# Performance work log

Measured on AMD Instinct MI355X. Metric: run time of the kernel, lower is better.

## Reference

```python
import jax, jax.numpy as jnp
import numpy as np

Y, Z, H, R = 32, 64, 256, 256  # y_dim, z_dim, h_dim, rnn_dim
T, B = 200, 2048


def setup_inputs() -> dict:
    key = jax.random.key(0)
    ks = jax.random.split(key, 32)
    w = lambda k, shape: jax.random.normal(k, shape, jnp.float32) * 0.05
    z32 = lambda n: jnp.zeros((n,), jnp.float32)
    return {
        "states": jax.random.normal(ks[0], (T, B, Y), jnp.float32),
        "eps": jax.random.normal(ks[1], (T - 1, B, Z), jnp.float32),
        # encoder q(z|x,y,h): Linear(2Y+R,H) ReLU Linear(H,H) ReLU
        "enc_w1": w(ks[2], (H, 2 * Y + R)), "enc_b1": z32(H),
        "enc_w2": w(ks[3], (H, H)), "enc_b2": z32(H),
        "enc_mw": w(ks[4], (Z, H)), "enc_mb": z32(Z),
        "enc_sw": w(ks[5], (Z, H)), "enc_sb": z32(Z),
        # prior p(z|y,h): Linear(Y+R,H) ReLU Linear(H,H) ReLU
        "pri_w1": w(ks[6], (H, Y + R)), "pri_b1": z32(H),
        "pri_w2": w(ks[7], (H, H)), "pri_b2": z32(H),
        "pri_mw": w(ks[8], (Z, H)), "pri_mb": z32(Z),
        "pri_sw": w(ks[9], (Z, H)), "pri_sb": z32(Z),
        # decoder p(x|y,z,h): Linear(Y+Z+R,H) ReLU Linear(H,H) ReLU
        "dec_w1": w(ks[10], (H, Y + Z + R)), "dec_b1": z32(H),
        "dec_w2": w(ks[11], (H, H)), "dec_b2": z32(H),
        "dec_mw": w(ks[12], (Y, H)), "dec_mb": z32(Y),
        "dec_sw": w(ks[13], (Y, H)), "dec_sb": z32(Y),
        # GRU(Y+Z -> R), 1 layer; torch gate order [r, z, n]
        "gru_wih": w(ks[14], (3 * R, Y + Z)), "gru_whh": w(ks[15], (3 * R, R)),
        "gru_bih": z32(3 * R), "gru_bhh": z32(3 * R),
    }


def reference(states, eps, enc_w1, enc_b1, enc_w2, enc_b2, enc_mw, enc_mb,
              enc_sw, enc_sb, pri_w1, pri_b1, pri_w2, pri_b2, pri_mw, pri_mb,
              pri_sw, pri_sb, dec_w1, dec_b1, dec_w2, dec_b2, dec_mw, dec_mb,
              dec_sw, dec_sb, gru_wih, gru_whh, gru_bih, gru_bhh):
    batch = states.shape[1]
    rnn_dim = gru_whh.shape[1]
    relu, sp = jax.nn.relu, jax.nn.softplus
    LOG2PI = jnp.float32(np.log(2.0 * np.pi))

    def mlp2(x, w1, b1, w2, b2):
        return relu(relu(x @ w1.T + b1) @ w2.T + b2)

    def step(h, inp):
        y, x, e = inp  # y=states[t], x=states[t+1], e: reparam noise
        enc_h = mlp2(jnp.concatenate([x, y, h], 1), enc_w1, enc_b1, enc_w2, enc_b2)
        em = enc_h @ enc_mw.T + enc_mb
        es = sp(enc_h @ enc_sw.T + enc_sb)
        pri_h = mlp2(jnp.concatenate([y, h], 1), pri_w1, pri_b1, pri_w2, pri_b2)
        pm = pri_h @ pri_mw.T + pri_mb
        ps = sp(pri_h @ pri_sw.T + pri_sb)
        z = em + es * e  # sample_gauss
        dec_h = mlp2(jnp.concatenate([y, z, h], 1), dec_w1, dec_b1, dec_w2, dec_b2)
        dm = dec_h @ dec_mw.T + dec_mb
        ds = sp(dec_h @ dec_sw.T + dec_sb)
        # GRU cell (torch gate order r,z,n)
        gi = jnp.concatenate([x, z], 1) @ gru_wih.T + gru_bih
        gh = h @ gru_whh.T + gru_bhh
        ir, iz, inn = jnp.split(gi, 3, axis=1)
        hr, hz, hn = jnp.split(gh, 3, axis=1)
        r = jax.nn.sigmoid(ir + hr)
        u = jax.nn.sigmoid(iz + hz)
        n = jnp.tanh(inn + r * hn)
        h_new = (1.0 - u) * n + u * h
        kl = 0.5 * jnp.sum(2.0 * jnp.log(ps / es) + (es ** 2 + (em - pm) ** 2) / ps ** 2 - 1.0)
        nll = jnp.sum(jnp.log(ds) + (x - dm) ** 2 / (2.0 * ds ** 2) + 0.5 * LOG2PI)
        return h_new, (kl, nll)

    h0 = jnp.zeros((batch, rnn_dim), states.dtype)
    _, (kls, nlls) = jax.lax.scan(step, h0, (states[:-1], states[1:], eps))
    # out = [kl_loss, recon_loss]
    return jnp.stack([jnp.sum(kls), jnp.sum(nlls)])
```

## Files before the change

kernel.cpp:

```cpp
#include <hip/hip_runtime.h>

typedef unsigned short u16;
typedef unsigned int u32;
typedef __bf16 bf16x8 __attribute__((ext_vector_type(8)));
typedef float f32x4 __attribute__((ext_vector_type(4)));

#define YD 32
#define ZD 64
#define HD 256
#define RD 256
#define TSTEPS 199
#define BB 2048
#define MROWS 32
#define NBLK 64
#define NTHR 1024
#define CATS 392
#define HBS  264
#define HES  136
#define HDS  72

enum : int {
  OFF_ENC_W1 = 0,
  OFF_ENC_W2 = 81920,
  OFF_ENC_H  = 147456,
  OFF_PRI_W1 = 180224,
  OFF_PRI_W2 = 253952,
  OFF_PRI_H  = 319488,
  OFF_DEC_W1 = 352256,
  OFF_DEC_W2 = 442368,
  OFF_DEC_H  = 507904,
  OFF_GWIH   = 524288,
  OFF_GWHH   = 598016,
};

__device__ __forceinline__ u16 f2bf(float f) {
  u32 u = __float_as_uint(f);
  u += 0x7fffu + ((u >> 16) & 1u);
  return (u16)(u >> 16);
}
__device__ __forceinline__ float bf2f(u16 b) {
  return __uint_as_float((u32)b << 16);
}
__device__ __forceinline__ float softplus_f(float x) {
  float l = __logf(1.f + __expf(-fabsf(x)));
  return x > 0.f ? x + l : l;
}
__device__ __forceinline__ float sigmoid_f(float x) {
  return __builtin_amdgcn_rcpf(1.f + __expf(-x));
}
__device__ __forceinline__ float tanh_f(float x) {
  float e = __expf(-2.f * fabsf(x));
  float t = (1.f - e) * __builtin_amdgcn_rcpf(1.f + e);
  return x >= 0.f ? t : -t;
}

template<int NT, int RT, int KS, int AS>
__device__ __forceinline__ void gemm_seg(f32x4 (&acc)[NT][RT],
    const u16* __restrict__ W, const int Kw, const int wrow0, const int wk0,
    const u16* A, const int acol0, const int rt0, const int lane)
{
  const int n = lane & 15, quad = lane >> 4;
  bf16x8 b[KS][NT];
  #pragma unroll
  for (int nt = 0; nt < NT; ++nt) {
    const u16* wp = W + (size_t)(wrow0 + nt * 16 + n) * Kw + wk0 + quad * 8;
    #pragma unroll
    for (int ks = 0; ks < KS; ++ks)
      b[ks][nt] = *reinterpret_cast<const bf16x8*>(wp + ks * 32);
  }
  #pragma unroll
  for (int ks = 0; ks < KS; ++ks) {
    bf16x8 a[RT];
    #pragma unroll
    for (int rt = 0; rt < RT; ++rt)
      a[rt] = *reinterpret_cast<const bf16x8*>(A + ((rt0 + rt) * 16 + n) * AS + acol0 + ks * 32 + quad * 8);
    #pragma unroll
    for (int nt = 0; nt < NT; ++nt)
      #pragma unroll
      for (int rt = 0; rt < RT; ++rt)
        acc[nt][rt] = __builtin_amdgcn_mfma_f32_16x16x32_bf16(a[rt], b[ks][nt], acc[nt][rt], 0, 0, 0);
  }
}

template<int RT, int DS>
__device__ __forceinline__ void store_relu(const f32x4 (&acc)[1][RT], u16* dst,
    const int col0, const int rt0, const float bias, const int lane)
{
  const int n = lane & 15, quad = lane >> 4;
  #pragma unroll
  for (int rt = 0; rt < RT; ++rt)
    #pragma unroll
    for (int i = 0; i < 4; ++i) {
      float v = fmaxf(acc[0][rt][i] + bias, 0.f);
      dst[((rt0 + rt) * 16 + quad * 4 + i) * DS + col0 + n] = f2bf(v);
    }
}

struct PrepArgs { const float* src[14]; int off[14]; int cnt[14]; };

__global__ void prep_weights(PrepArgs a, u16* __restrict__ dst) {
  const int j = blockIdx.y;
  const float* __restrict__ s = a.src[j];
  u16* d = dst + a.off[j];
  const int nel = a.cnt[j];
  for (int i = blockIdx.x * blockDim.x + threadIdx.x; i < nel; i += gridDim.x * blockDim.x)
    d[i] = f2bf(s[i]);
}

__global__ void zero_out_k(float* out) { if (threadIdx.x < 2) out[threadIdx.x] = 0.f; }

__global__ __launch_bounds__(NTHR, 4)
void vrnn_kernel(const float* __restrict__ states, const float* __restrict__ eps,
                 const float* __restrict__ enc_b1, const float* __restrict__ enc_b2,
                 const float* __restrict__ enc_mb, const float* __restrict__ enc_sb,
                 const float* __restrict__ pri_b1, const float* __restrict__ pri_b2,
                 const float* __restrict__ pri_mb, const float* __restrict__ pri_sb,
                 const float* __restrict__ dec_b1, const float* __restrict__ dec_b2,
                 const float* __restrict__ dec_mb, const float* __restrict__ dec_sb,
                 const float* __restrict__ gbih, const float* __restrict__ gbhh,
                 const u16* __restrict__ ws, float* __restrict__ out)
{
  __shared__ u16 cat[MROWS * CATS];
  __shared__ u16 hb1[MROWS * HBS];
  __shared__ u16 hb2[MROWS * HBS];
  __shared__ u16 hbhE[MROWS * HES];
  __shared__ u16 hbhP[MROWS * HES];
  __shared__ u16 hbhD[MROWS * HDS];

  const int tid = threadIdx.x;
  const int w = tid >> 6, lane = tid & 63;
  const int n = lane & 15, quad = lane >> 4;
  const int r0 = blockIdx.x * MROWS;
  const int n0 = w * 16;
  const int cgE = w & 7, rtE = w >> 3;
  const int cgD = w & 3, rtD = (w >> 2) & 1;

  const int jW = n0 + n;
  const float b1e = enc_b1[jW], b2e = enc_b2[jW];
  const float b1p = pri_b1[jW], b2p = pri_b2[jW];
  const float b1d = dec_b1[jW], b2d = dec_b2[jW];
  const float brg = gbih[jW] + gbhh[jW];
  const float bug = gbih[RD + jW] + gbhh[RD + jW];
  const float bing = gbih[2 * RD + jW];
  const float bhng = gbhh[2 * RD + jW];
  const float bhE = (cgE < 4) ? enc_mb[cgE * 16 + n] : enc_sb[(cgE - 4) * 16 + n];
  const float bhP = (cgE < 4) ? pri_mb[cgE * 16 + n] : pri_sb[(cgE - 4) * 16 + n];
  const float bhD = (cgD < 2) ? dec_mb[cgD * 16 + n] : dec_sb[(cgD - 2) * 16 + n];

  for (int i = tid; i < MROWS * (HD / 2); i += NTHR) {
    int row = i >> 7, c = (i & 127) * 2;
    *reinterpret_cast<u32*>(&cat[row * CATS + 128 + c]) = 0u;
  }

  float hreg[2][4];
  #pragma unroll
  for (int a = 0; a < 2; ++a)
    #pragma unroll
    for (int c = 0; c < 4; ++c) hreg[a][c] = 0.f;

  const int srow = (tid & 255) >> 3, sc4 = (tid & 7) * 4;
  float4 xyf = make_float4(0.f, 0.f, 0.f, 0.f);
  if (tid < 512)
    xyf = *reinterpret_cast<const float4*>(states + ((size_t)((tid < 256) ? 1 : 0) * BB + r0 + srow) * YD + sc4);

  const int mz = tid >> 5, jz = (tid & 31) * 2;
  const int mn = (tid & 511) >> 4, jn = (tid & 15) * 2;

  float kl_acc = 0.f, nll_acc = 0.f;

  for (int t = 0; t < TSTEPS; ++t) {
    if (tid < 512) {
      u16* d = cat + srow * CATS + ((tid < 256) ? 0 : 32) + sc4;
      d[0] = f2bf(xyf.x); d[1] = f2bf(xyf.y); d[2] = f2bf(xyf.z); d[3] = f2bf(xyf.w);
    }
    float2 ev2 = *reinterpret_cast<const float2*>(eps + ((size_t)t * BB + r0 + mz) * ZD + jz);
    float2 xs2 = make_float2(0.f, 0.f);
    if (tid < 512)
      xs2 = *reinterpret_cast<const float2*>(states + ((size_t)(t + 1) * BB + r0 + mn) * YD + jn);
    __syncthreads();

    {
      f32x4 acc[1][2] = {};
      gemm_seg<1, 2, 2, CATS>(acc, ws + OFF_ENC_W1, 320, n0, 0, cat, 0, 0, lane);
      gemm_seg<1, 2, 8, CATS>(acc, ws + OFF_ENC_W1, 320, n0, 64, cat, 128, 0, lane);
      store_relu<2, HBS>(acc, hb1, n0, 0, b1e, lane);
    }
    __syncthreads();

    {
      f32x4 acc[1][2] = {};
      gemm_seg<1, 2, 8, HBS>(acc, ws + OFF_ENC_W2, 256, n0, 0, hb1, 0, 0, lane);
      store_relu<2, HBS>(acc, hb2, n0, 0, b2e, lane);
    }
    __syncthreads();

    {
      f32x4 acc[1][1] = {};
      gemm_seg<1, 1, 8, HBS>(acc, ws + OFF_ENC_H, 256, cgE * 16, 0, hb2, 0, rtE, lane);
      #pragma unroll
      for (int i = 0; i < 4; ++i) {
        float v = acc[0][0][i] + bhE;
        if (cgE >= 4) v = softplus_f(v);
        hbhE[(rtE * 16 + quad * 4 + i) * HES + cgE * 16 + n] = f2bf(v);
      }
    }
    __syncthreads();

    {
      float em0 = bf2f(hbhE[mz * HES + jz]);
      float em1 = bf2f(hbhE[mz * HES + jz + 1]);
      float es0 = bf2f(hbhE[mz * HES + 64 + jz]);
      float es1 = bf2f(hbhE[mz * HES + 64 + jz + 1]);
      cat[mz * CATS + 64 + jz] = f2bf(em0 + es0 * ev2.x);
      cat[mz * CATS + 64 + jz + 1] = f2bf(em1 + es1 * ev2.y);
      f32x4 acc[1][2] = {};
      gemm_seg<1, 2, 1, CATS>(acc, ws + OFF_PRI_W1, 288, n0, 0, cat, 32, 0, lane);
      gemm_seg<1, 2, 8, CATS>(acc, ws + OFF_PRI_W1, 288, n0, 32, cat, 128, 0, lane);
      store_relu<2, HBS>(acc, hb1, n0, 0, b1p, lane);
    }
    __syncthreads();

    {
      f32x4 acc[1][2] = {};
      gemm_seg<1, 2, 8, HBS>(acc, ws + OFF_PRI_W2, 256, n0, 0, hb1, 0, 0, lane);
      store_relu<2, HBS>(acc, hb2, n0, 0, b2p, lane);
    }
    __syncthreads();

    {
      f32x4 acc[1][1] = {};
      gemm_seg<1, 1, 8, HBS>(acc, ws + OFF_PRI_H, 256, cgE * 16, 0, hb2, 0, rtE, lane);
      #pragma unroll
      for (int i = 0; i < 4; ++i) {
        float v = acc[0][0][i] + bhP;
        if (cgE >= 4) v = softplus_f(v);
        hbhP[(rtE * 16 + quad * 4 + i) * HES + cgE * 16 + n] = f2bf(v);
      }
    }
    __syncthreads();

    {
      #pragma unroll
      for (int c = 0; c < 2; ++c) {
        float em = bf2f(hbhE[mz * HES + jz + c]);
        float es = bf2f(hbhE[mz * HES + 64 + jz + c]);
        float pm = bf2f(hbhP[mz * HES + jz + c]);
        float ps = bf2f(hbhP[mz * HES + 64 + jz + c]);
        float d = em - pm;
        kl_acc += 0.5f * (2.f * __logf(ps * __builtin_amdgcn_rcpf(es))
                          + (es * es + d * d) / (ps * ps) - 1.f);
      }
      f32x4 acc[1][2] = {};
      gemm_seg<1, 2, 3, CATS>(acc, ws + OFF_DEC_W1, 352, n0, 0, cat, 32, 0, lane);
      gemm_seg<1, 2, 8, CATS>(acc, ws + OFF_DEC_W1, 352, n0, 96, cat, 128, 0, lane);
      store_relu<2, HBS>(acc, hb1, n0, 0, b1d, lane);
    }
    __syncthreads();

    {
      f32x4 acc[1][2] = {};
      gemm_seg<1, 2, 8, HBS>(acc, ws + OFF_DEC_W2, 256, n0, 0, hb1, 0, 0, lane);
      store_relu<2, HBS>(acc, hb2, n0, 0, b2d, lane);
    }
    __syncthreads();

    {
      if (w < 8) {
        f32x4 acc[1][1] = {};
        gemm_seg<1, 1, 8, HBS>(acc, ws + OFF_DEC_H, 256, cgD * 16, 0, hb2, 0, rtD, lane);
        #pragma unroll
        for (int i = 0; i < 4; ++i) {
          float v = acc[0][0][i] + bhD;
          if (cgD >= 2) v = softplus_f(v);
          hbhD[(rtD * 16 + quad * 4 + i) * HDS + cgD * 16 + n] = f2bf(v);
        }
      }
      f32x4 aH[1][2] = {};
      gemm_seg<1, 2, 8, CATS>(aH, ws + OFF_GWHH, 256, 2 * RD + n0, 0, cat, 128, 0, lane);
      {
        f32x4 aR[1][2] = {};
        gemm_seg<1, 2, 1, CATS>(aR, ws + OFF_GWIH, 96, n0, 0, cat, 0, 0, lane);
        gemm_seg<1, 2, 2, CATS>(aR, ws + OFF_GWIH, 96, n0, 32, cat, 64, 0, lane);
        gemm_seg<1, 2, 8, CATS>(aR, ws + OFF_GWHH, 256, n0, 0, cat, 128, 0, lane);
        #pragma unroll
        for (int rt = 0; rt < 2; ++rt)
          #pragma unroll
          for (int i = 0; i < 4; ++i)
            aH[0][rt][i] = sigmoid_f(aR[0][rt][i] + brg) * (aH[0][rt][i] + bhng);
      }
      {
        f32x4 aN[1][2] = {};
        gemm_seg<1, 2, 1, CATS>(aN, ws + OFF_GWIH, 96, 2 * RD + n0, 0, cat, 0, 0, lane);
        gemm_seg<1, 2, 2, CATS>(aN, ws + OFF_GWIH, 96, 2 * RD + n0, 32, cat, 64, 0, lane);
        #pragma unroll
        for (int rt = 0; rt < 2; ++rt)
          #pragma unroll
          for (int i = 0; i < 4; ++i)
            aH[0][rt][i] = tanh_f(aN[0][rt][i] + bing + aH[0][rt][i]);
      }
      {
        f32x4 aU[1][2] = {};
        gemm_seg<1, 2, 1, CATS>(aU, ws + OFF_GWIH, 96, RD + n0, 0, cat, 0, 0, lane);
        gemm_seg<1, 2, 2, CATS>(aU, ws + OFF_GWIH, 96, RD + n0, 32, cat, 64, 0, lane);
        gemm_seg<1, 2, 8, CATS>(aU, ws + OFF_GWHH, 256, RD + n0, 0, cat, 128, 0, lane);
        #pragma unroll
        for (int rt = 0; rt < 2; ++rt)
          #pragma unroll
          for (int i = 0; i < 4; ++i) {
            float u = sigmoid_f(aU[0][rt][i] + bug);
            hreg[rt][i] = (1.f - u) * aH[0][rt][i] + u * hreg[rt][i];
          }
      }
      const int tn = (t + 1 < TSTEPS) ? t + 1 : TSTEPS - 1;
      if (tid < 512)
        xyf = *reinterpret_cast<const float4*>(states + ((size_t)((tid < 256) ? tn + 1 : tn) * BB + r0 + srow) * YD + sc4);
    }
    __syncthreads();

    if (tid < 512) {
      #pragma unroll
      for (int c = 0; c < 2; ++c) {
        float dm = bf2f(hbhD[mn * HDS + jn + c]);
        float ds = bf2f(hbhD[mn * HDS + 32 + jn + c]);
        float xv = (c == 0) ? xs2.x : xs2.y;
        float dd = xv - dm;
        nll_acc += __logf(ds) + dd * dd / (2.f * ds * ds) + 0.91893853320467274178f;
      }
    }
    #pragma unroll
    for (int rt = 0; rt < 2; ++rt)
      #pragma unroll
      for (int i = 0; i < 4; ++i)
        cat[(rt * 16 + quad * 4 + i) * CATS + 128 + n0 + n] = f2bf(hreg[rt][i]);
  }

  float kv = kl_acc, nv = nll_acc;
  #pragma unroll
  for (int off = 32; off > 0; off >>= 1) {
    kv += __shfl_down(kv, off, 64);
    nv += __shfl_down(nv, off, 64);
  }
  if (lane == 0) {
    atomicAdd(out + 0, kv);
    atomicAdd(out + 1, nv);
  }
}

extern "C" void kernel_launch(void* const* d_in, const int* in_sizes, int n_in,
                              void* d_out, int out_size, void* d_ws, size_t ws_size,
                              hipStream_t stream) {
  const float* states = (const float*)d_in[0];
  const float* eps    = (const float*)d_in[1];
  u16* ws   = (u16*)d_ws;
  float* out = (float*)d_out;

  PrepArgs pa;
  const int jsrc[14] = {2, 4, 6, 8, 10, 12, 14, 16, 18, 20, 22, 24, 26, 27};
  const int joff[14] = {OFF_ENC_W1, OFF_ENC_W2, OFF_ENC_H, OFF_ENC_H + 16384,
                        OFF_PRI_W1, OFF_PRI_W2, OFF_PRI_H, OFF_PRI_H + 16384,
                        OFF_DEC_W1, OFF_DEC_W2, OFF_DEC_H, OFF_DEC_H + 8192,
                        OFF_GWIH, OFF_GWHH};
  const int jcnt[14] = {81920, 65536, 16384, 16384,
                        73728, 65536, 16384, 16384,
                        90112, 65536, 8192, 8192,
                        73728, 196608};
  for (int j = 0; j < 14; ++j) {
    pa.src[j] = (const float*)d_in[jsrc[j]];
    pa.off[j] = joff[j];
    pa.cnt[j] = jcnt[j];
  }

  zero_out_k<<<dim3(1), dim3(64), 0, stream>>>(out);
  prep_weights<<<dim3(64, 14), dim3(256), 0, stream>>>(pa, ws);
  vrnn_kernel<<<dim3(NBLK), dim3(NTHR), 0, stream>>>(
      states, eps,
      (const float*)d_in[3],  (const float*)d_in[5],
      (const float*)d_in[7],  (const float*)d_in[9],
      (const float*)d_in[11], (const float*)d_in[13],
      (const float*)d_in[15], (const float*)d_in[17],
      (const float*)d_in[19], (const float*)d_in[21],
      (const float*)d_in[23], (const float*)d_in[25],
      (const float*)d_in[28], (const float*)d_in[29],
      ws, out);
}
```

Measured before the change: 10.77 ms.

## Process 64 batch rows per block to double weight reuse per MFMA fragment

Each block now handles 64 batch rows instead of 32, so each loaded weight fragment feeds four MFMA row tiles instead of two, halving the global/L2 weight traffic per row. Grid shrinks to 32 blocks, the LDS padding strides change, and the decoder-head buffer is folded into hb1 to fit the larger tiles in LDS. Input loads become nontemporal, and all threads now take part in staging states, eps and the NLL terms. With 32 blocks on a many-CU GPU, far fewer compute units are busy, which may outweigh the reuse gain.

```diff
diff --git a/kernel.cpp b/kernel.cpp
--- a/kernel.cpp
+++ b/kernel.cpp
@@ -4,6 +4,7 @@
 typedef unsigned int u32;
 typedef __bf16 bf16x8 __attribute__((ext_vector_type(8)));
 typedef float f32x4 __attribute__((ext_vector_type(4)));
+typedef float f32x2 __attribute__((ext_vector_type(2)));
 
 #define YD 32
 #define ZD 64
@@ -11,13 +12,12 @@
 #define RD 256
 #define TSTEPS 199
 #define BB 2048
-#define MROWS 32
-#define NBLK 64
+#define MROWS 64
+#define NBLK 32
 #define NTHR 1024
-#define CATS 392
-#define HBS  264
-#define HES  136
-#define HDS  72
+#define CATS 388
+#define HBS  260
+#define HES  132
 
 enum : int {
   OFF_ENC_W1 = 0,
@@ -54,36 +54,29 @@
   return x >= 0.f ? t : -t;
 }
 
-template<int NT, int RT, int KS, int AS>
-__device__ __forceinline__ void gemm_seg(f32x4 (&acc)[NT][RT],
+template<int RT, int KS, int AS>
+__device__ __forceinline__ void gemm_seg(f32x4 (&acc)[RT],
     const u16* __restrict__ W, const int Kw, const int wrow0, const int wk0,
     const u16* A, const int acol0, const int rt0, const int lane)
 {
   const int n = lane & 15, quad = lane >> 4;
-  bf16x8 b[KS][NT];
-  #pragma unroll
-  for (int nt = 0; nt < NT; ++nt) {
-    const u16* wp = W + (size_t)(wrow0 + nt * 16 + n) * Kw + wk0 + quad * 8;
+  bf16x8 b[KS];
+  const u16* wp = W + (size_t)(wrow0 + n) * Kw + wk0 + quad * 8;
+  #pragma unroll
+  for (int ks = 0; ks < KS; ++ks)
+    b[ks] = *reinterpret_cast<const bf16x8*>(wp + ks * 32);
+  #pragma unroll
+  for (int ks = 0; ks < KS; ++ks) {
     #pragma unroll
-    for (int ks = 0; ks < KS; ++ks)
-      b[ks][nt] = *reinterpret_cast<const bf16x8*>(wp + ks * 32);
-  }
-  #pragma unroll
-  for (int ks = 0; ks < KS; ++ks) {
-    bf16x8 a[RT];
-    #pragma unroll
-    for (int rt = 0; rt < RT; ++rt)
-      a[rt] = *reinterpret_cast<const bf16x8*>(A + ((rt0 + rt) * 16 + n) * AS + acol0 + ks * 32 + quad * 8);
-    #pragma unroll
-    for (int nt = 0; nt < NT; ++nt)
-      #pragma unroll
-      for (int rt = 0; rt < RT; ++rt)
-        acc[nt][rt] = __builtin_amdgcn_mfma_f32_16x16x32_bf16(a[rt], b[ks][nt], acc[nt][rt], 0, 0, 0);
+    for (int rt = 0; rt < RT; ++rt) {
+      bf16x8 a = *reinterpret_cast<const bf16x8*>(A + ((rt0 + rt) * 16 + n) * AS + acol0 + ks * 32 + quad * 8);
+      acc[rt] = __builtin_amdgcn_mfma_f32_16x16x32_bf16(a, b[ks], acc[rt], 0, 0, 0);
+    }
   }
 }
 
 template<int RT, int DS>
-__device__ __forceinline__ void store_relu(const f32x4 (&acc)[1][RT], u16* dst,
+__device__ __forceinline__ void store_relu(const f32x4 (&acc)[RT], u16* dst,
     const int col0, const int rt0, const float bias, const int lane)
 {
   const int n = lane & 15, quad = lane >> 4;
@@ -91,7 +84,7 @@
   for (int rt = 0; rt < RT; ++rt)
     #pragma unroll
     for (int i = 0; i < 4; ++i) {
-      float v = fmaxf(acc[0][rt][i] + bias, 0.f);
+      float v = fmaxf(acc[rt][i] + bias, 0.f);
       dst[((rt0 + rt) * 16 + quad * 4 + i) * DS + col0 + n] = f2bf(v);
     }
 }
@@ -125,15 +118,14 @@
   __shared__ u16 hb2[MROWS * HBS];
   __shared__ u16 hbhE[MROWS * HES];
   __shared__ u16 hbhP[MROWS * HES];
-  __shared__ u16 hbhD[MROWS * HDS];
 
   const int tid = threadIdx.x;
   const int w = tid >> 6, lane = tid & 63;
   const int n = lane & 15, quad = lane >> 4;
   const int r0 = blockIdx.x * MROWS;
   const int n0 = w * 16;
-  const int cgE = w & 7, rtE = w >> 3;
-  const int cgD = w & 3, rtD = (w >> 2) & 1;
+  const int cgE = w & 7, rtE0 = (w >> 3) * 2;
+  const int cgD = w & 3, rtD = w >> 2;
 
   const int jW = n0 + n;
   const float b1e = enc_b1[jW], b2e = enc_b2[jW];
@@ -152,96 +144,100 @@
     *reinterpret_cast<u32*>(&cat[row * CATS + 128 + c]) = 0u;
   }
 
-  float hreg[2][4];
-  #pragma unroll
-  for (int a = 0; a < 2; ++a)
+  float hreg[4][4];
+  #pragma unroll
+  for (int a = 0; a < 4; ++a)
     #pragma unroll
     for (int c = 0; c < 4; ++c) hreg[a][c] = 0.f;
 
-  const int srow = (tid & 255) >> 3, sc4 = (tid & 7) * 4;
-  float4 xyf = make_float4(0.f, 0.f, 0.f, 0.f);
-  if (tid < 512)
-    xyf = *reinterpret_cast<const float4*>(states + ((size_t)((tid < 256) ? 1 : 0) * BB + r0 + srow) * YD + sc4);
-
-  const int mz = tid >> 5, jz = (tid & 31) * 2;
-  const int mn = (tid & 511) >> 4, jn = (tid & 15) * 2;
+  const int srow = (tid & 511) >> 3, sc4 = (tid & 7) * 4;
+  f32x4 xyf = __builtin_nontemporal_load(
+      reinterpret_cast<const f32x4*>(states + ((size_t)((tid < 512) ? 1 : 0) * BB + r0 + srow) * YD + sc4));
+
+  const int mz = tid >> 4, jz = (tid & 15) * 4;
+  const int mn = tid >> 4, jn = (tid & 15) * 2;
 
   float kl_acc = 0.f, nll_acc = 0.f;
 
   for (int t = 0; t < TSTEPS; ++t) {
-    if (tid < 512) {
-      u16* d = cat + srow * CATS + ((tid < 256) ? 0 : 32) + sc4;
+    {
+      u16* d = cat + srow * CATS + ((tid < 512) ? 0 : 32) + sc4;
       d[0] = f2bf(xyf.x); d[1] = f2bf(xyf.y); d[2] = f2bf(xyf.z); d[3] = f2bf(xyf.w);
     }
-    float2 ev2 = *reinterpret_cast<const float2*>(eps + ((size_t)t * BB + r0 + mz) * ZD + jz);
-    float2 xs2 = make_float2(0.f, 0.f);
-    if (tid < 512)
-      xs2 = *reinterpret_cast<const float2*>(states + ((size_t)(t + 1) * BB + r0 + mn) * YD + jn);
-    __syncthreads();
-
-    {
-      f32x4 acc[1][2] = {};
-      gemm_seg<1, 2, 2, CATS>(acc, ws + OFF_ENC_W1, 320, n0, 0, cat, 0, 0, lane);
-      gemm_seg<1, 2, 8, CATS>(acc, ws + OFF_ENC_W1, 320, n0, 64, cat, 128, 0, lane);
-      store_relu<2, HBS>(acc, hb1, n0, 0, b1e, lane);
-    }
-    __syncthreads();
-
-    {
-      f32x4 acc[1][2] = {};
-      gemm_seg<1, 2, 8, HBS>(acc, ws + OFF_ENC_W2, 256, n0, 0, hb1, 0, 0, lane);
-      store_relu<2, HBS>(acc, hb2, n0, 0, b2e, lane);
-    }
-    __syncthreads();
-
-    {
-      f32x4 acc[1][1] = {};
-      gemm_seg<1, 1, 8, HBS>(acc, ws + OFF_ENC_H, 256, cgE * 16, 0, hb2, 0, rtE, lane);
-      #pragma unroll
-      for (int i = 0; i < 4; ++i) {
-        float v = acc[0][0][i] + bhE;
-        if (cgE >= 4) v = softplus_f(v);
-        hbhE[(rtE * 16 + quad * 4 + i) * HES + cgE * 16 + n] = f2bf(v);
-      }
-    }
-    __syncthreads();
-
-    {
-      float em0 = bf2f(hbhE[mz * HES + jz]);
-      float em1 = bf2f(hbhE[mz * HES + jz + 1]);
-      float es0 = bf2f(hbhE[mz * HES + 64 + jz]);
-      float es1 = bf2f(hbhE[mz * HES + 64 + jz + 1]);
-      cat[mz * CATS + 64 + jz] = f2bf(em0 + es0 * ev2.x);
-      cat[mz * CATS + 64 + jz + 1] = f2bf(em1 + es1 * ev2.y);
-      f32x4 acc[1][2] = {};
-      gemm_seg<1, 2, 1, CATS>(acc, ws + OFF_PRI_W1, 288, n0, 0, cat, 32, 0, lane);
-      gemm_seg<1, 2, 8, CATS>(acc, ws + OFF_PRI_W1, 288, n0, 32, cat, 128, 0, lane);
-      store_relu<2, HBS>(acc, hb1, n0, 0, b1p, lane);
-    }
-    __syncthreads();
-
-    {
-      f32x4 acc[1][2] = {};
-      gemm_seg<1, 2, 8, HBS>(acc, ws + OFF_PRI_W2, 256, n0, 0, hb1, 0, 0, lane);
-      store_relu<2, HBS>(acc, hb2, n0, 0, b2p, lane);
-    }
-    __syncthreads();
-
-    {
-      f32x4 acc[1][1] = {};
-      gemm_seg<1, 1, 8, HBS>(acc, ws + OFF_PRI_H, 256, cgE * 16, 0, hb2, 0, rtE, lane);
-      #pragma unroll
-      for (int i = 0; i < 4; ++i) {
-        float v = acc[0][0][i] + bhP;
-        if (cgE >= 4) v = softplus_f(v);
-        hbhP[(rtE * 16 + quad * 4 + i) * HES + cgE * 16 + n] = f2bf(v);
-      }
-    }
-    __syncthreads();
-
-    {
-      #pragma unroll
-      for (int c = 0; c < 2; ++c) {
+    f32x4 ev4 = __builtin_nontemporal_load(
+        reinterpret_cast<const f32x4*>(eps + ((size_t)t * BB + r0 + mz) * ZD + jz));
+    f32x2 xs2 = __builtin_nontemporal_load(
+        reinterpret_cast<const f32x2*>(states + ((size_t)(t + 1) * BB + r0 + mn) * YD + jn));
+    __syncthreads();
+
+    {
+      f32x4 acc[4] = {};
+      gemm_seg<4, 2, CATS>(acc, ws + OFF_ENC_W1, 320, n0, 0, cat, 0, 0, lane);
+      gemm_seg<4, 8, CATS>(acc, ws + OFF_ENC_W1, 320, n0, 64, cat, 128, 0, lane);
+      store_relu<4, HBS>(acc, hb1, n0, 0, b1e, lane);
+    }
+    __syncthreads();
+
+    {
+      f32x4 acc[4] = {};
+      gemm_seg<4, 8, HBS>(acc, ws + OFF_ENC_W2, 256, n0, 0, hb1, 0, 0, lane);
+      store_relu<4, HBS>(acc, hb2, n0, 0, b2e, lane);
+    }
+    __syncthreads();
+
+    {
+      f32x4 acc[2] = {};
+      gemm_seg<2, 8, HBS>(acc, ws + OFF_ENC_H, 256, cgE * 16, 0, hb2, 0, rtE0, lane);
+      #pragma unroll
+      for (int rt = 0; rt < 2; ++rt)
+        #pragma unroll
+        for (int i = 0; i < 4; ++i) {
+          float v = acc[rt][i] + bhE;
+          if (cgE >= 4) v = softplus_f(v);
+          hbhE[((rtE0 + rt) * 16 + quad * 4 + i) * HES + cgE * 16 + n] = f2bf(v);
+        }
+    }
+    __syncthreads();
+
+    {
+      const float e4[4] = {ev4.x, ev4.y, ev4.z, ev4.w};
+      #pragma unroll
+      for (int c = 0; c < 4; ++c) {
+        float em = bf2f(hbhE[mz * HES + jz + c]);
+        float es = bf2f(hbhE[mz * HES + 64 + jz + c]);
+        cat[mz * CATS + 64 + jz + c] = f2bf(em + es * e4[c]);
+      }
+      f32x4 acc[4] = {};
+      gemm_seg<4, 1, CATS>(acc, ws + OFF_PRI_W1, 288, n0, 0, cat, 32, 0, lane);
+      gemm_seg<4, 8, CATS>(acc, ws + OFF_PRI_W1, 288, n0, 32, cat, 128, 0, lane);
+      store_relu<4, HBS>(acc, hb1, n0, 0, b1p, lane);
+    }
+    __syncthreads();
+
+    {
+      f32x4 acc[4] = {};
+      gemm_seg<4, 8, HBS>(acc, ws + OFF_PRI_W2, 256, n0, 0, hb1, 0, 0, lane);
+      store_relu<4, HBS>(acc, hb2, n0, 0, b2p, lane);
+    }
+    __syncthreads();
+
+    {
+      f32x4 acc[2] = {};
+      gemm_seg<2, 8, HBS>(acc, ws + OFF_PRI_H, 256, cgE * 16, 0, hb2, 0, rtE0, lane);
+      #pragma unroll
+      for (int rt = 0; rt < 2; ++rt)
+        #pragma unroll
+        for (int i = 0; i < 4; ++i) {
+          float v = acc[rt][i] + bhP;
+          if (cgE >= 4) v = softplus_f(v);
+          hbhP[((rtE0 + rt) * 16 + quad * 4 + i) * HES + cgE * 16 + n] = f2bf(v);
+        }
+    }
+    __syncthreads();
+
+    {
+      #pragma unroll
+      for (int c = 0; c < 4; ++c) {
         float em = bf2f(hbhE[mz * HES + jz + c]);
         float es = bf2f(hbhE[mz * HES + 64 + jz + c]);
         float pm = bf2f(hbhP[mz * HES + jz + c]);
@@ -250,85 +246,85 @@
         kl_acc += 0.5f * (2.f * __logf(ps * __builtin_amdgcn_rcpf(es))
                           + (es * es + d * d) / (ps * ps) - 1.f);
       }
-      f32x4 acc[1][2] = {};
-      gemm_seg<1, 2, 3, CATS>(acc, ws + OFF_DEC_W1, 352, n0, 0, cat, 32, 0, lane);
-      gemm_seg<1, 2, 8, CATS>(acc, ws + OFF_DEC_W1, 352, n0, 96, cat, 128, 0, lane);
-      store_relu<2, HBS>(acc, hb1, n0, 0, b1d, lane);
-    }
-    __syncthreads();
-
-    {
-      f32x4 acc[1][2] = {};
-      gemm_seg<1, 2, 8, HBS>(acc, ws + OFF_DEC_W2, 256, n0, 0, hb1, 0, 0, lane);
-      store_relu<2, HBS>(acc, hb2, n0, 0, b2d, lane);
-    }
-    __syncthreads();
-
-    {
-      if (w < 8) {
-        f32x4 acc[1][1] = {};
-        gemm_seg<1, 1, 8, HBS>(acc, ws + OFF_DEC_H, 256, cgD * 16, 0, hb2, 0, rtD, lane);
+      f32x4 acc[4] = {};
+      gemm_seg<4, 3, CATS>(acc, ws + OFF_DEC_W1, 352, n0, 0, cat, 32, 0, lane);
+      gemm_seg<4, 8, CATS>(acc, ws + OFF_DEC_W1, 352, n0, 96, cat, 128, 0, lane);
+      store_relu<4, HBS>(acc, hb1, n0, 0, b1d, lane);
+    }
+    __syncthreads();
+
+    {
+      f32x4 acc[4] = {};
+      gemm_seg<4, 8, HBS>(acc, ws + OFF_DEC_W2, 256, n0, 0, hb1, 0, 0, lane);
+      store_relu<4, HBS>(acc, hb2, n0, 0, b2d, lane);
+    }
+    __syncthreads();
+
+    {
+      {
+        f32x4 acc[1] = {};
+        gemm_seg<1, 8, HBS>(acc, ws + OFF_DEC_H, 256, cgD * 16, 0, hb2, 0, rtD, lane);
         #pragma unroll
         for (int i = 0; i < 4; ++i) {
-          float v = acc[0][0][i] + bhD;
+          float v = acc[0][i] + bhD;
           if (cgD >= 2) v = softplus_f(v);
-          hbhD[(rtD * 16 + quad * 4 + i) * HDS + cgD * 16 + n] = f2bf(v);
+          hb1[(rtD * 16 + quad * 4 + i) * HBS + cgD * 16 + n] = f2bf(v);
         }
       }
-      f32x4 aH[1][2] = {};
-      gemm_seg<1, 2, 8, CATS>(aH, ws + OFF_GWHH, 256, 2 * RD + n0, 0, cat, 128, 0, lane);
+      f32x4 aH[4] = {};
+      gemm_seg<4, 8, CATS>(aH, ws + OFF_GWHH, 256, 2 * RD + n0, 0, cat, 128, 0, lane);
       {
-        f32x4 aR[1][2] = {};
-        gemm_seg<1, 2, 1, CATS>(aR, ws + OFF_GWIH, 96, n0, 0, cat, 0, 0, lane);
-        gemm_seg<1, 2, 2, CATS>(aR, ws + OFF_GWIH, 96, n0, 32, cat, 64, 0, lane);
-        gemm_seg<1, 2, 8, CATS>(aR, ws + OFF_GWHH, 256, n0, 0, cat, 128, 0, lane);
-        #pragma unroll
-        for (int rt = 0; rt < 2; ++rt)
+        f32x4 aR[4] = {};
+        gemm_seg<4, 1, CATS>(aR, ws + OFF_GWIH, 96, n0, 0, cat, 0, 0, lane);
+        gemm_seg<4, 2, CATS>(aR, ws + OFF_GWIH, 96, n0, 32, cat, 64, 0, lane);
+        gemm_seg<4, 8, CATS>(aR, ws + OFF_GWHH, 256, n0, 0, cat, 128, 0, lane);
+        #pragma unroll
+        for (int rt = 0; rt < 4; ++rt)
           #pragma unroll
           for (int i = 0; i < 4; ++i)
-            aH[0][rt][i] = sigmoid_f(aR[0][rt][i] + brg) * (aH[0][rt][i] + bhng);
+            aH[rt][i] = sigmoid_f(aR[rt][i] + brg) * (aH[rt][i] + bhng);
       }
       {
-        f32x4 aN[1][2] = {};
-        gemm_seg<1, 2, 1, CATS>(aN, ws + OFF_GWIH, 96, 2 * RD + n0, 0, cat, 0, 0, lane);
-        gemm_seg<1, 2, 2, CATS>(aN, ws + OFF_GWIH, 96, 2 * RD + n0, 32, cat, 64, 0, lane);
-        #pragma unroll
-        for (int rt = 0; rt < 2; ++rt)
+        f32x4 aN[4] = {};
+        gemm_seg<4, 1, CATS>(aN, ws + OFF_GWIH, 96, 2 * RD + n0, 0, cat, 0, 0, lane);
+        gemm_seg<4, 2, CATS>(aN, ws + OFF_GWIH, 96, 2 * RD + n0, 32, cat, 64, 0, lane);
+        #pragma unroll
+        for (int rt = 0; rt < 4; ++rt)
           #pragma unroll
           for (int i = 0; i < 4; ++i)
-            aH[0][rt][i] = tanh_f(aN[0][rt][i] + bing + aH[0][rt][i]);
+            aH[rt][i] = tanh_f(aN[rt][i] + bing + aH[rt][i]);
       }
       {
-        f32x4 aU[1][2] = {};
-        gemm_seg<1, 2, 1, CATS>(aU, ws + OFF_GWIH, 96, RD + n0, 0, cat, 0, 0, lane);
-        gemm_seg<1, 2, 2, CATS>(aU, ws + OFF_GWIH, 96, RD + n0, 32, cat, 64, 0, lane);
-        gemm_seg<1, 2, 8, CATS>(aU, ws + OFF_GWHH, 256, RD + n0, 0, cat, 128, 0, lane);
-        #pragma unroll
-        for (int rt = 0; rt < 2; ++rt)
+        f32x4 aU[4] = {};
+        gemm_seg<4, 1, CATS>(aU, ws + OFF_GWIH, 96, RD + n0, 0, cat, 0, 0, lane);
+        gemm_seg<4, 2, CATS>(aU, ws + OFF_GWIH, 96, RD + n0, 32, cat, 64, 0, lane);
+        gemm_seg<4, 8, CATS>(aU, ws + OFF_GWHH, 256, RD + n0, 0, cat, 128, 0, lane);
+        #pragma unroll
+        for (int rt = 0; rt < 4; ++rt)
           #pragma unroll
           for (int i = 0; i < 4; ++i) {
-            float u = sigmoid_f(aU[0][rt][i] + bug);
-            hreg[rt][i] = (1.f - u) * aH[0][rt][i] + u * hreg[rt][i];
+            float u = sigmoid_f(aU[rt][i] + bug);
+            hreg[rt][i] = (1.f - u) * aH[rt][i] + u * hreg[rt][i];
           }
       }
       const int tn = (t + 1 < TSTEPS) ? t + 1 : TSTEPS - 1;
-      if (tid < 512)
-        xyf = *reinterpret_cast<const float4*>(states + ((size_t)((tid < 256) ? tn + 1 : tn) * BB + r0 + srow) * YD + sc4);
-    }
-    __syncthreads();
-
-    if (tid < 512) {
+      xyf = __builtin_nontemporal_load(
+          reinterpret_cast<const f32x4*>(states + ((size_t)((tid < 512) ? tn + 1 : tn) * BB + r0 + srow) * YD + sc4));
+    }
+    __syncthreads();
+
+    {
+      const float x2[2] = {xs2.x, xs2.y};
       #pragma unroll
       for (int c = 0; c < 2; ++c) {
-        float dm = bf2f(hbhD[mn * HDS + jn + c]);
-        float ds = bf2f(hbhD[mn * HDS + 32 + jn + c]);
-        float xv = (c == 0) ? xs2.x : xs2.y;
-        float dd = xv - dm;
+        float dm = bf2f(hb1[mn * HBS + jn + c]);
+        float ds = bf2f(hb1[mn * HBS + 32 + jn + c]);
+        float dd = x2[c] - dm;
         nll_acc += __logf(ds) + dd * dd / (2.f * ds * ds) + 0.91893853320467274178f;
       }
     }
     #pragma unroll
-    for (int rt = 0; rt < 2; ++rt)
+    for (int rt = 0; rt < 4; ++rt)
       #pragma unroll
       for (int i = 0; i < 4; ++i)
         cat[(rt * 16 + quad * 4 + i) * CATS + 128 + n0 + n] = f2bf(hreg[rt][i]);
```

New measurement: 33.51 ms. +211.1%, slower.
